# Kernel optimization log

Hardware: AMD Instinct MI355X
Metric: run time of the kernel (lower is better)

Reference implementation:

```python
import jax, jax.numpy as jnp
import numpy as np

DIM = 2048
NUM_EXPERTS = 64
K = 2


def setup_inputs() -> dict:
    key = jax.random.key(0)
    kx, kw, kb = jax.random.split(key, 3)
    x = jax.random.normal(kx, (4, 8192, DIM), dtype=jnp.float32)
    # nn.Linear(dim, num_experts): weight [E, dim], bias [E]
    bound = 1.0 / np.sqrt(DIM)
    W = jax.random.uniform(kw, (NUM_EXPERTS, DIM), minval=-bound, maxval=bound, dtype=jnp.float32)
    b = jax.random.uniform(kb, (NUM_EXPERTS,), minval=-bound, maxval=bound, dtype=jnp.float32)
    return {"x": x, "W": W, "b": b}


def reference(x, W, b):
    # gate_logits = x @ W.T + b  -> [B, S, E]
    gate_logits = jnp.einsum("bsd,ed->bse", x, W) + b
    gate_scores = jax.nn.softmax(gate_logits, axis=-1)
    topk_scores, topk_idx = jax.lax.top_k(gate_scores, K)  # [B, S, K]
    return gate_scores, topk_idx, topk_scores
```

## Files before the change

### kernel.cpp

```cpp
#include <hip/hip_runtime.h>
#include <hip/hip_bf16.h>
#include <stdint.h>
#include <stddef.h>

#define DIM   2048
#define NEXP  64
#define NTOK  32768
#define KF    64
#define OFF_IDX  (NTOK*NEXP)
#define OFF_TSC  (OFF_IDX + NTOK*2)
#define TAU   5e-4f

typedef __attribute__((ext_vector_type(8))) short  short8;
typedef __attribute__((ext_vector_type(4))) float  f32x4;

__device__ __forceinline__ unsigned short bf16_rne(float f) {
    unsigned u = __builtin_bit_cast(unsigned, f);
    u += 0x7fffu + ((u >> 16) & 1u);
    return (unsigned short)(u >> 16);
}
__device__ __forceinline__ float bf16_up(unsigned short s) {
    unsigned u = ((unsigned)s) << 16;
    return __builtin_bit_cast(float, u);
}

__global__ __launch_bounds__(256) void wsplit(const float* __restrict__ W,
                                              short* __restrict__ warr,
                                              int* __restrict__ cnt) {
    int idx  = blockIdx.x * 256 + threadIdx.x;
    if (idx == 0) *cnt = 0;
    int j    = idx & 7;
    int lane = (idx >> 3) & 63;
    int nf   = (idx >> 9) & 3;
    int kf   = (idx >> 11) & 63;
    int term = idx >> 17;
    int e = nf * 16 + (lane & 15);
    int d = kf * 32 + (lane >> 4) * 8 + j;
    float w = W[e * DIM + d];
    unsigned short h  = bf16_rne(w);
    float r1 = w - bf16_up(h);
    unsigned short md = bf16_rne(r1);
    warr[idx] = (short)((term == 0) ? h : md);
}

__device__ __forceinline__ bool gtie(float a, int ia, float b, int ib) {
    return (a > b) || (a == b && ia < ib);
}

__global__ __launch_bounds__(512, 4) void router_mfma(
        const float* __restrict__ X, const short* __restrict__ Wsp,
        const float* __restrict__ bias, float* __restrict__ out,
        int* __restrict__ cnt, int* __restrict__ list) {
    __shared__ char smem[65536] __attribute__((aligned(16)));
    const int tid  = threadIdx.x;
    const int lane = tid & 63;
    const int w    = tid >> 6;
    const int wq   = w & 3;
    const int kh   = w >> 2;
    const int tok0 = blockIdx.x * 64 + wq * 16;
    const int l15  = lane & 15;
    const int l4   = lane >> 4;

    const int q2  = tid >> 7;
    const int khs = q2 >> 1, ts = q2 & 1;
    const int li  = tid & 127;
    const char* wsrc = (const char*)Wsp + ((size_t)ts * 64 + khs * 32) * 4096 + li * 16;
    char* bdst = smem + q2 * 16384 + li * 16;

    const float* xr = X + (size_t)(tok0 + l15) * DIM + kh * 1024 + l4 * 8;
    const char*  bq = smem + (kh * 2) * 16384 + lane * 16;

    f32x4 acc[4];
#pragma unroll
    for (int n = 0; n < 4; n++) acc[n] = (f32x4)0.0f;

    f32x4 a_pf[2][2];
#pragma unroll
    for (int p = 0; p < 2; p++) {
        a_pf[p][0] = *(const f32x4*)(xr + p * 32);
        a_pf[p][1] = *(const f32x4*)(xr + p * 32 + 4);
    }

#pragma unroll 1
    for (int g = 0; g < 8; ++g) {
        __syncthreads();
        {
            const char* s0 = wsrc + g * 16384;
            f32x4 ld[8];
#pragma unroll
            for (int i = 0; i < 8; i++) ld[i] = *(const f32x4*)(s0 + i * 2048);
#pragma unroll
            for (int i = 0; i < 8; i++) *(f32x4*)(bdst + i * 2048) = ld[i];
        }
        __syncthreads();

#pragma unroll
        for (int p = 0; p < 4; ++p) {
            const int lkf = g * 4 + p;
            const int kn  = (lkf + 2 < 32) ? lkf + 2 : 31;
            const int s   = p & 1;

            f32x4 a0 = a_pf[s][0], a1 = a_pf[s][1];
            a_pf[s][0] = *(const f32x4*)(xr + kn * 32);
            a_pf[s][1] = *(const f32x4*)(xr + kn * 32 + 4);

            short8 b[2][4];
#pragma unroll
            for (int t = 0; t < 2; t++)
#pragma unroll
                for (int n = 0; n < 4; n++)
                    b[t][n] = *(const short8*)(bq + t * 16384 + p * 4096 + n * 1024);

            short8 ah, am;
#pragma unroll
            for (int j = 0; j < 8; j++) {
                float v = (j < 4) ? a0[j & 3] : a1[j & 3];
                unsigned short h  = bf16_rne(v);
                float r1 = v - bf16_up(h);
                unsigned short md = bf16_rne(r1);
                ah[j] = (short)h;
                am[j] = (short)md;
            }

#pragma unroll
            for (int n = 0; n < 4; n++) {
                f32x4 c = acc[n];
                c = __builtin_amdgcn_mfma_f32_16x16x32_bf16(ah, b[0][n], c, 0, 0, 0);
                c = __builtin_amdgcn_mfma_f32_16x16x32_bf16(ah, b[1][n], c, 0, 0, 0);
                c = __builtin_amdgcn_mfma_f32_16x16x32_bf16(am, b[0][n], c, 0, 0, 0);
                c = __builtin_amdgcn_mfma_f32_16x16x32_bf16(am, b[1][n], c, 0, 0, 0);
                acc[n] = c;
            }
        }
    }

    __syncthreads();
    if (kh == 1) {
#pragma unroll
        for (int n = 0; n < 4; n++)
            *(f32x4*)(smem + ((size_t)(wq * 4 + n)) * 1024 + lane * 16) = acc[n];
    }
    __syncthreads();
    if (kh == 1) return;
#pragma unroll
    for (int n = 0; n < 4; n++)
        acc[n] += *(const f32x4*)(smem + ((size_t)(wq * 4 + n)) * 1024 + lane * 16);

    float bv[4];
#pragma unroll
    for (int n = 0; n < 4; n++) bv[n] = bias[n * 16 + l15];

#pragma unroll
    for (int r = 0; r < 4; r++) {
        const int t = tok0 + l4 * 4 + r;
        float v[4];
#pragma unroll
        for (int n = 0; n < 4; n++) v[n] = acc[n][r] + bv[n];

        float mx = fmaxf(fmaxf(v[0], v[1]), fmaxf(v[2], v[3]));
#pragma unroll
        for (int s = 1; s < 16; s <<= 1) mx = fmaxf(mx, __shfl_xor(mx, s, 64));

        float p[4], den = 0.0f;
#pragma unroll
        for (int n = 0; n < 4; n++) { p[n] = __expf(v[n] - mx); den += p[n]; }
#pragma unroll
        for (int s = 1; s < 16; s <<= 1) den += __shfl_xor(den, s, 64);
        const float inv = 1.0f / den;
#pragma unroll
        for (int n = 0; n < 4; n++)
            out[(size_t)t * 64 + n * 16 + l15] = p[n] * inv;

        float v1 = -3.4e38f, v2 = -3.4e38f, v3 = -3.4e38f;
        int   i1 = 9999,     i2 = 9999,     i3 = 9999;
#pragma unroll
        for (int n = 0; n < 4; n++) {
            float vv = v[n]; int ii = n * 16 + l15;
            if (gtie(vv, ii, v1, i1))      { v3=v2;i3=i2; v2=v1;i2=i1; v1=vv;i1=ii; }
            else if (gtie(vv, ii, v2, i2)) { v3=v2;i3=i2; v2=vv;i2=ii; }
            else if (gtie(vv, ii, v3, i3)) { v3=vv;i3=ii; }
        }
#pragma unroll
        for (int s = 1; s < 16; s <<= 1) {
            float ov1=__shfl_xor(v1,s,64), ov2=__shfl_xor(v2,s,64), ov3=__shfl_xor(v3,s,64);
            int   oi1=__shfl_xor(i1,s,64), oi2=__shfl_xor(i2,s,64), oi3=__shfl_xor(i3,s,64);
            bool a1 = gtie(v1,i1,ov1,oi1);
            float w1 = a1?v1:ov1;  int k1 = a1?i1:oi1;
            float x1 = a1?v2:ov2;  int xi1= a1?i2:oi2;
            float x2 = a1?v3:ov3;  int xi2= a1?i3:oi3;
            float y1 = a1?ov1:v1;  int yi1= a1?oi1:i1;
            float y2 = a1?ov2:v2;  int yi2= a1?oi2:i2;
            bool a2 = gtie(x1,xi1,y1,yi1);
            float w2 = a2?x1:y1;   int k2 = a2?xi1:yi1;
            float w3; int k3;
            if (a2) { bool a3 = gtie(x2,xi2,y1,yi1); w3 = a3?x2:y1; k3 = a3?xi2:yi1; }
            else    { bool a3 = gtie(x1,xi1,y2,yi2); w3 = a3?x1:y2; k3 = a3?xi1:yi2; }
            v1=w1;i1=k1; v2=w2;i2=k2; v3=w3;i3=k3;
        }
        if (l15 == 0) {
            out[OFF_IDX + (size_t)t * 2 + 0] = (float)i1;
            out[OFF_IDX + (size_t)t * 2 + 1] = (float)i2;
            out[OFF_TSC + (size_t)t * 2 + 0] = __expf(v1 - mx) * inv;
            out[OFF_TSC + (size_t)t * 2 + 1] = __expf(v2 - mx) * inv;
            if ((v1 - v2 < TAU) || (v2 - v3 < TAU)) {
                int slot = atomicAdd(cnt, 1);
                list[slot] = t;
            }
        }
    }
}

__global__ __launch_bounds__(256, 2) void router_exact(
        const float* __restrict__ X, const float* __restrict__ W,
        const float* __restrict__ Bb, float* __restrict__ out,
        const int* __restrict__ cnt, const int* __restrict__ list) {
    __shared__ float xrow[2048];
    __shared__ char  wbuf[2][64 * 272] __attribute__((aligned(16)));
    const int tid = threadIdx.x;
    const int n   = *cnt;

    for (int ii = blockIdx.x; ii < n; ii += gridDim.x) {
        const int t = list[ii];
#pragma unroll
        for (int q = 0; q < 2; ++q) {
            int s = tid + q * 256;
            *(f32x4*)&xrow[s * 4] = *(const f32x4*)(X + (size_t)t * DIM + s * 4);
        }
#pragma unroll
        for (int q = 0; q < 4; ++q) {
            int s = tid + q * 256;
            int e = s >> 4, dq = s & 15;
            f32x4 wv = *(const f32x4*)(W + (size_t)e * DIM + dq * 4);
            *(f32x4*)(wbuf[0] + e * 272 + ((16 * dq) ^ ((e & 7) << 4))) = wv;
        }
        __syncthreads();

        float acc = 0.0f;
#pragma unroll 1
        for (int c = 0; c < 32; ++c) {
            if (c + 1 < 32) {
#pragma unroll
                for (int q = 0; q < 4; ++q) {
                    int s = tid + q * 256;
                    int e = s >> 4, dq = s & 15;
                    f32x4 wv = *(const f32x4*)(W + (size_t)e * DIM + (c + 1) * 64 + dq * 4);
                    *(f32x4*)(wbuf[(c + 1) & 1] + e * 272 + ((16 * dq) ^ ((e & 7) << 4))) = wv;
                }
            }
            if (tid < 64) {
                const char* wb = wbuf[c & 1] + tid * 272;
                const int sw = (tid & 7) << 4;
#pragma unroll
                for (int dq = 0; dq < 16; ++dq) {
                    f32x4 xq = *(const f32x4*)&xrow[c * 64 + dq * 4];
                    f32x4 wv = *(const f32x4*)(wb + ((16 * dq) ^ sw));
#pragma unroll
                    for (int j = 0; j < 4; ++j)
                        acc = fmaf(xq[j], wv[j], acc);
                }
            }
            __syncthreads();
        }

        if (tid < 64) {
            const int lane = tid;
            const float lg = acc + Bb[lane];
            float m = lg;
#pragma unroll
            for (int s = 1; s < 64; s <<= 1) m = fmaxf(m, __shfl_xor(m, s, 64));
            const float p = __expf(lg - m);
            float den = p;
#pragma unroll
            for (int s = 1; s < 64; s <<= 1) den += __shfl_xor(den, s, 64);
            const float inv = 1.0f / den;
            out[(size_t)t * 64 + lane] = p * inv;

            float v1 = lg, v2 = -3.4e38f;
            int   i1 = lane, i2 = 127;
#pragma unroll
            for (int s = 1; s < 64; s <<= 1) {
                float ov1 = __shfl_xor(v1, s, 64), ov2 = __shfl_xor(v2, s, 64);
                int   oi1 = __shfl_xor(i1, s, 64), oi2 = __shfl_xor(i2, s, 64);
                bool  aw  = gtie(v1, i1, ov1, oi1);
                float nv1 = aw ? v1 : ov1;  int ni1 = aw ? i1 : oi1;
                float cv  = aw ? ov1 : v1;  int ci  = aw ? oi1 : i1;
                float sv  = aw ? v2 : ov2;  int si  = aw ? i2 : oi2;
                bool  c2  = gtie(cv, ci, sv, si);
                v1 = nv1; i1 = ni1;
                v2 = c2 ? cv : sv; i2 = c2 ? ci : si;
            }
            if (lane == 0) {
                out[OFF_IDX + (size_t)t * 2 + 0] = (float)i1;
                out[OFF_IDX + (size_t)t * 2 + 1] = (float)i2;
                out[OFF_TSC + (size_t)t * 2 + 0] = __expf(v1 - m) * inv;
                out[OFF_TSC + (size_t)t * 2 + 1] = __expf(v2 - m) * inv;
            }
        }
        __syncthreads();
    }
}

extern "C" void kernel_launch(void* const* d_in, const int* in_sizes, int n_in,
                              void* d_out, int out_size, void* d_ws, size_t ws_size,
                              hipStream_t stream) {
    const float* X = (const float*)d_in[0];
    const float* W = (const float*)d_in[1];
    const float* b = (const float*)d_in[2];
    float* out  = (float*)d_out;
    short* Wsp  = (short*)d_ws;
    int*   cnt  = (int*)((char*)d_ws + 524288);
    int*   list = (int*)((char*)d_ws + 524292);

    wsplit<<<1024, 256, 0, stream>>>(W, Wsp, cnt);
    router_mfma<<<NTOK / 64, 512, 0, stream>>>(X, Wsp, b, out, cnt, list);
    router_exact<<<512, 256, 0, stream>>>(X, W, b, out, cnt, list);
}
```

Before: 98.25 us.

## Stage X tiles through swizzled LDS with register-prefetched W/X double pipeline

Replaces direct per-lane global loads of X with cooperative coalesced loads into an XOR-swizzled shared-memory tile, and splits the W staging into 16 smaller chunks. Each iteration prefetches the next X and W chunk into registers before computing on the current one, then writes them to LDS after a barrier. This aims to coalesce X reads and hide global latency, at the cost of two barriers per chunk and extra LDS traffic.

```diff
diff --git a/kernel.cpp b/kernel.cpp
--- a/kernel.cpp
+++ b/kernel.cpp
@@ -6,7 +6,6 @@
 #define DIM   2048
 #define NEXP  64
 #define NTOK  32768
-#define KF    64
 #define OFF_IDX  (NTOK*NEXP)
 #define OFF_TSC  (OFF_IDX + NTOK*2)
 #define TAU   5e-4f
@@ -57,59 +56,84 @@
     const int w    = tid >> 6;
     const int wq   = w & 3;
     const int kh   = w >> 2;
-    const int tok0 = blockIdx.x * 64 + wq * 16;
+    const int tokb = blockIdx.x * 64;
+    const int tok0 = tokb + wq * 16;
     const int l15  = lane & 15;
     const int l4   = lane >> 4;
 
-    const int q2  = tid >> 7;
-    const int khs = q2 >> 1, ts = q2 & 1;
-    const int li  = tid & 127;
-    const char* wsrc = (const char*)Wsp + ((size_t)ts * 64 + khs * 32) * 4096 + li * 16;
-    char* bdst = smem + q2 * 16384 + li * 16;
-
-    const float* xr = X + (size_t)(tok0 + l15) * DIM + kh * 1024 + l4 * 8;
-    const char*  bq = smem + (kh * 2) * 16384 + lane * 16;
+    const int srow0 = (w & 3) * 16 + l4;
+    const int sslot = l15;
+    const char* wbytes = (const char*)Wsp;
+
+    const int arow = wq * 16 + l15;
+    const int asw  = (l15 & 7) << 4;
 
     f32x4 acc[4];
 #pragma unroll
     for (int n = 0; n < 4; n++) acc[n] = (f32x4)0.0f;
 
-    f32x4 a_pf[2][2];
-#pragma unroll
-    for (int p = 0; p < 2; p++) {
-        a_pf[p][0] = *(const f32x4*)(xr + p * 32);
-        a_pf[p][1] = *(const f32x4*)(xr + p * 32 + 4);
-    }
+    {
+        f32x4 xst[4], bst[4];
+#pragma unroll
+        for (int i = 0; i < 4; i++) {
+            const int r = srow0 + i * 4;
+            xst[i] = *(const f32x4*)(X + (size_t)(tokb + r) * DIM + kh * 1024 + sslot * 4);
+        }
+#pragma unroll
+        for (int j = 0; j < 4; j++) {
+            const int u   = tid * 64 + j * 16;
+            const int pi  = u >> 12;
+            const int inn = u & 4095;
+            const int term = pi >> 2, kh2 = (pi >> 1) & 1, pk = pi & 1;
+            const int kfs  = kh2 * 32 + 0 * 2 + pk;
+            bst[j] = *(const f32x4*)(wbytes + ((size_t)(term * 64 + kfs)) * 4096 + inn);
+        }
+#pragma unroll
+        for (int i = 0; i < 4; i++) {
+            const int r = srow0 + i * 4;
+            *(f32x4*)(smem + kh * 16384 + r * 256 + ((sslot * 16) ^ ((r & 7) << 4))) = xst[i];
+        }
+#pragma unroll
+        for (int j = 0; j < 4; j++)
+            *(f32x4*)(smem + 32768 + tid * 64 + j * 16) = bst[j];
+    }
+    __syncthreads();
 
 #pragma unroll 1
-    for (int g = 0; g < 8; ++g) {
-        __syncthreads();
-        {
-            const char* s0 = wsrc + g * 16384;
-            f32x4 ld[8];
-#pragma unroll
-            for (int i = 0; i < 8; i++) ld[i] = *(const f32x4*)(s0 + i * 2048);
-#pragma unroll
-            for (int i = 0; i < 8; i++) *(f32x4*)(bdst + i * 2048) = ld[i];
-        }
-        __syncthreads();
-
-#pragma unroll
-        for (int p = 0; p < 4; ++p) {
-            const int lkf = g * 4 + p;
-            const int kn  = (lkf + 2 < 32) ? lkf + 2 : 31;
-            const int s   = p & 1;
-
-            f32x4 a0 = a_pf[s][0], a1 = a_pf[s][1];
-            a_pf[s][0] = *(const f32x4*)(xr + kn * 32);
-            a_pf[s][1] = *(const f32x4*)(xr + kn * 32 + 4);
+    for (int g = 0; g < 16; ++g) {
+        f32x4 xst[4], bst[4];
+        if (g < 15) {
+#pragma unroll
+            for (int i = 0; i < 4; i++) {
+                const int r = srow0 + i * 4;
+                xst[i] = *(const f32x4*)(X + (size_t)(tokb + r) * DIM + kh * 1024
+                                         + (g + 1) * 64 + sslot * 4);
+            }
+#pragma unroll
+            for (int j = 0; j < 4; j++) {
+                const int u   = tid * 64 + j * 16;
+                const int pi  = u >> 12;
+                const int inn = u & 4095;
+                const int term = pi >> 2, kh2 = (pi >> 1) & 1, pk = pi & 1;
+                const int kfs  = kh2 * 32 + (g + 1) * 2 + pk;
+                bst[j] = *(const f32x4*)(wbytes + ((size_t)(term * 64 + kfs)) * 4096 + inn);
+            }
+            __builtin_amdgcn_sched_barrier(0);
+        }
+
+#pragma unroll
+        for (int p = 0; p < 2; ++p) {
+            const int s16 = (p * 8 + l4 * 2) * 16;
+            f32x4 a0 = *(const f32x4*)(smem + kh * 16384 + arow * 256 + ((s16)      ^ asw));
+            f32x4 a1 = *(const f32x4*)(smem + kh * 16384 + arow * 256 + ((s16 + 16) ^ asw));
 
             short8 b[2][4];
 #pragma unroll
             for (int t = 0; t < 2; t++)
 #pragma unroll
                 for (int n = 0; n < 4; n++)
-                    b[t][n] = *(const short8*)(bq + t * 16384 + p * 4096 + n * 1024);
+                    b[t][n] = *(const short8*)(smem + 32768 + (t * 4 + kh * 2 + p) * 4096
+                                               + n * 1024 + lane * 16);
 
             short8 ah, am;
 #pragma unroll
@@ -132,9 +156,21 @@
                 acc[n] = c;
             }
         }
-    }
-
-    __syncthreads();
+
+        __syncthreads();
+        if (g < 15) {
+#pragma unroll
+            for (int i = 0; i < 4; i++) {
+                const int r = srow0 + i * 4;
+                *(f32x4*)(smem + kh * 16384 + r * 256 + ((sslot * 16) ^ ((r & 7) << 4))) = xst[i];
+            }
+#pragma unroll
+            for (int j = 0; j < 4; j++)
+                *(f32x4*)(smem + 32768 + tid * 64 + j * 16) = bst[j];
+        }
+        __syncthreads();
+    }
+
     if (kh == 1) {
 #pragma unroll
         for (int n = 0; n < 4; n++)
```

New measurement: 103.0 us. 4.8% more time.
